# Optimization experiments

Measured on AMD Instinct MI355X. Metric: run time of the kernel, lower is better.

## Reference

```python
import jax, jax.numpy as jnp
import numpy as np

TEMPERATURE = 0.1
NEG_INF = -1e9


def setup_inputs() -> dict:
    key = jax.random.key(0)
    k1, k2 = jax.random.split(key)
    features = jax.random.normal(k1, (8192, 256), dtype=jnp.float32)
    labels = jax.random.randint(k2, (4096, 1), 0, 1000, dtype=jnp.int64)
    return {"features": features, "labels": labels}


def reference(features, labels):
    N = features.shape[0]
    n_views = N // labels.shape[0]
    # labels repeated over views: [N, 1]
    labels_nv = jnp.tile(labels, (n_views, 1))
    eye = jnp.eye(N, dtype=bool)
    # contrastive mask: 1 where same class, 0 on diagonal
    mask = (labels_nv == labels_nv.T).astype(features.dtype)
    mask = jnp.where(eye, 0.0, mask)
    # pairwise similarity logits [N, N], diagonal masked out
    logits = jnp.matmul(features, features.T) / TEMPERATURE
    logits = jnp.where(eye, NEG_INF, logits)
    # NOTE: torch code divides by mask.sum(dim=1) WITHOUT keepdim, which
    # broadcasts over the last axis (divide by column's row-sum). mask is
    # symmetric so this equals per-row normalization; replicate exactly.
    soft_label = mask / mask.sum(axis=1)
    log_proba = jax.nn.log_softmax(logits, axis=-1)
    loss_all = jnp.sum(soft_label * log_proba, axis=-1)  # [N]
    loss = -jnp.mean(loss_all) * TEMPERATURE
    return loss
```

## Files before the change

### kernel.cpp

```cpp
#include <hip/hip_runtime.h>

typedef __bf16 bf16_t;
typedef bf16_t bf16x8 __attribute__((ext_vector_type(8)));
typedef float f32x4 __attribute__((ext_vector_type(4)));
typedef unsigned short ushort_t;
typedef unsigned int uint_t;

#define C10L2E 14.4269504088896340736f
#define LN2    0.69314718055994530942f
#define NEG_BIG -3.0e38f
#define M0     -1.0e30f
#define THR_L2 11.5415603f

static __device__ __forceinline__ float fexp2(float x){ return __builtin_amdgcn_exp2f(x); }
static __device__ __forceinline__ float flog2(float x){ return __builtin_amdgcn_logf(x); }

#define GLOAD16(g, l) __builtin_amdgcn_global_load_lds( \
    (const __attribute__((address_space(1))) void*)(g), \
    (__attribute__((address_space(3))) void*)(l), 16, 0, 0)

#define WAITV(n) asm volatile("s_waitcnt vmcnt(" #n ")" ::: "memory")

static __device__ __forceinline__ ushort_t f2bf1(float f) {
    uint_t u = __float_as_uint(f);
    uint_t r = (u + 0x7fffu + ((u >> 16) & 1u)) >> 16;
    return (ushort_t)r;
}

__global__ void prep_kernel(const float* __restrict__ feat, const int* __restrict__ labels,
                            ushort_t* __restrict__ Fb, int* __restrict__ cnt,
                            int* __restrict__ idxl) {
    int i = blockIdx.x * 256 + threadIdx.x;
    float4 f = reinterpret_cast<const float4*>(feat)[i];
    ushort4 o;
    o.x = f2bf1(f.x); o.y = f2bf1(f.y); o.z = f2bf1(f.z); o.w = f2bf1(f.w);
    reinterpret_cast<ushort4*>(Fb)[i] = o;
    if (i < 4096) {
        int lab = labels[i];
        int p = atomicAdd(&cnt[lab], 1);
        if (p < 64) idxl[lab * 64 + p] = i;
    }
}

__global__ void classterm_kernel(const float* __restrict__ feat, const int* __restrict__ cnt,
                                 const int* __restrict__ idxl, float* __restrict__ term) {
    int c = blockIdx.x;
    int lane = threadIdx.x;
    int n = cnt[c];
    float4 g4 = make_float4(0.f, 0.f, 0.f, 0.f);
    float n2 = 0.f;
    for (int e = 0; e < n; ++e) {
        int r = idxl[c * 64 + e];
        float4 f0 = reinterpret_cast<const float4*>(feat)[(size_t)r * 64 + lane];
        float4 f1 = reinterpret_cast<const float4*>(feat)[(size_t)(r + 4096) * 64 + lane];
        g4.x += f0.x + f1.x; g4.y += f0.y + f1.y;
        g4.z += f0.z + f1.z; g4.w += f0.w + f1.w;
        n2 += f0.x*f0.x + f0.y*f0.y + f0.z*f0.z + f0.w*f0.w
            + f1.x*f1.x + f1.y*f1.y + f1.z*f1.z + f1.w*f1.w;
    }
    float gg = g4.x*g4.x + g4.y*g4.y + g4.z*g4.z + g4.w*g4.w;
    #pragma unroll
    for (int d = 1; d < 64; d <<= 1) {
        gg += __shfl_xor(gg, d, 64);
        n2 += __shfl_xor(n2, d, 64);
    }
    if (lane == 0) term[c] = (n > 0) ? (gg - n2) / (float)(2 * n - 1) : 0.0f;
}

__global__ __launch_bounds__(512, 1) void supcon_main(
        const ushort_t* __restrict__ Fb, float* __restrict__ part) {
    extern __shared__ char lds[];
    char* As = lds;
    char* Bb = lds + 65536;

    const int tid  = threadIdx.x;
    const int lane = tid & 63;
    const int wid  = tid >> 6;
    const int wr   = (wid >> 2) * 64;
    const int wc   = (wid & 3) * 64;
    const int g    = lane >> 4;
    const int l15  = lane & 15;
    const int r0 = blockIdx.x * 128;
    const int c0 = blockIdx.y * 2048;

    #pragma unroll
    for (int i = 0; i < 8; ++i) {
        int c = (wid * 8 + i) * 64 + lane;
        int row = c >> 5, sl = c & 31;
        int lslot = (sl & 16) | ((sl ^ row) & 15);
        GLOAD16(Fb + (size_t)(r0 + row) * 256 + lslot * 8, As + c * 16);
    }

    int bofs0, bofs1, bdst0, bdst1;
    {
        int c = tid;
        int col = c >> 2, pp = c & 3;
        bofs0 = col * 256 + (pp ^ ((col >> 1) & 3)) * 8;
        bdst0 = c * 16;
        c = 512 + tid;
        col = c >> 2; pp = c & 3;
        bofs1 = col * 256 + (pp ^ ((col >> 1) & 3)) * 8;
        bdst1 = c * 16;
    }
    auto stageB = [&](int p) {
        const ushort_t* base = Fb + (size_t)(c0 + (p >> 3) * 256) * 256 + (p & 7) * 32;
        char* Bd = Bb + (p & 3) * 16384;
        GLOAD16(base + bofs0, Bd + bdst0);
        GLOAD16(base + bofs1, Bd + bdst1);
    };

    stageB(0); stageB(1);

    float ML2[16], S[16];
    #pragma unroll
    for (int x = 0; x < 16; ++x) { ML2[x] = M0; S[x] = 0.0f; }

    f32x4 acc[4][4];

    #pragma unroll 1
    for (int t = 0; t < 8; ++t) {
        const int j0 = c0 + t * 256;
        #pragma unroll
        for (int e = 0; e < 8; ++e) {
            const int p = t * 8 + e;
            if (e <= 5) {
                stageB(p + 2);
                WAITV(4);
            } else if (e == 6) {
                if (t < 7) { stageB(p + 2); WAITV(4); } else { WAITV(2); }
            } else {
                if (t < 7) { stageB(p + 2); WAITV(4); } else { WAITV(0); }
            }
            __builtin_amdgcn_s_barrier();
            __builtin_amdgcn_sched_barrier(0);

            bf16x8 a[4], b[4];
            {
                int sA = e * 4 + g;
                int pA = (sA & 16) | ((sA ^ l15) & 15);
                #pragma unroll
                for (int m = 0; m < 4; ++m)
                    a[m] = *reinterpret_cast<const bf16x8*>(As + (wr + m * 16 + l15) * 512 + pA * 16);
                const char* Bp = Bb + (p & 3) * 16384;
                int pB = g ^ ((l15 >> 1) & 3);
                #pragma unroll
                for (int n = 0; n < 4; ++n)
                    b[n] = *reinterpret_cast<const bf16x8*>(Bp + (wc + n * 16 + l15) * 64 + pB * 16);
            }

            if (e == 0) {
                #pragma unroll
                for (int m = 0; m < 4; ++m)
                    #pragma unroll
                    for (int n = 0; n < 4; ++n)
                        #pragma unroll
                        for (int w = 0; w < 4; ++w) acc[m][n][w] = 0.0f;
            }
            #pragma unroll
            for (int m = 0; m < 4; ++m)
                #pragma unroll
                for (int n = 0; n < 4; ++n)
                    acc[m][n] = __builtin_amdgcn_mfma_f32_16x16x32_bf16(a[m], b[n], acc[m][n], 0, 0, 0);

            if (e == 7) {
                const bool diag = (j0 == (r0 & ~255));
                const int jc = j0 + wc + l15;
                #pragma unroll
                for (int m = 0; m < 4; ++m) {
                    #pragma unroll
                    for (int v = 0; v < 4; ++v) {
                        const int idx = m * 4 + v;
                        float x0 = acc[m][0][v], x1 = acc[m][1][v];
                        float x2 = acc[m][2][v], x3 = acc[m][3][v];
                        if (diag) {
                            int i = r0 + wr + m * 16 + g * 4 + v;
                            if (jc      == i) x0 = NEG_BIG;
                            if (jc + 16 == i) x1 = NEG_BIG;
                            if (jc + 32 == i) x2 = NEG_BIG;
                            if (jc + 48 == i) x3 = NEG_BIG;
                        }
                        float tm = fmaxf(fmaxf(x0, x1), fmaxf(x2, x3));
                        float cc = tm * C10L2E;
                        float ml = ML2[idx];
                        if (cc > ml + THR_L2) {
                            S[idx] *= fexp2(ml - cc);
                            ml = cc;
                            ML2[idx] = cc;
                        }
                        S[idx] += fexp2(fmaf(x0, C10L2E, -ml)) + fexp2(fmaf(x1, C10L2E, -ml))
                                + fexp2(fmaf(x2, C10L2E, -ml)) + fexp2(fmaf(x3, C10L2E, -ml));
                    }
                }
            }
        }
    }

    const int slot = blockIdx.y * 4 + (wid & 3);
    #pragma unroll
    for (int idx = 0; idx < 16; ++idx) {
        float m_ = ML2[idx], s_ = S[idx];
        #pragma unroll
        for (int d = 1; d < 16; d <<= 1) {
            float mo = __shfl_xor(m_, d, 64);
            float so = __shfl_xor(s_, d, 64);
            float nm = fmaxf(m_, mo);
            s_ = s_ * fexp2(m_ - nm) + so * fexp2(mo - nm);
            m_ = nm;
        }
        if (l15 == 0) {
            int i = r0 + wr + (idx >> 2) * 16 + g * 4 + (idx & 3);
            float2 val; val.x = m_; val.y = s_;
            *reinterpret_cast<float2*>(part + ((size_t)i * 16 + slot) * 2) = val;
        }
    }
}

__global__ void combine_kernel(const float* __restrict__ part, const float* __restrict__ term,
                               float* __restrict__ acc, int* __restrict__ cntr,
                               float* __restrict__ out) {
    __shared__ float sm[16];
    int tid = threadIdx.x;
    int row = blockIdx.x * 16 + (tid >> 4);
    int l16 = tid & 15;
    float2 v = reinterpret_cast<const float2*>(part)[(size_t)row * 16 + l16];
    float m_ = v.x, s_ = v.y;
    #pragma unroll
    for (int d = 1; d < 16; d <<= 1) {
        float mo = __shfl_xor(m_, d, 64);
        float so = __shfl_xor(s_, d, 64);
        float nm = fmaxf(m_, mo);
        s_ = s_ * fexp2(m_ - nm) + so * fexp2(mo - nm);
        m_ = nm;
    }
    if (l16 == 0) sm[tid >> 4] = LN2 * (m_ + flog2(s_));
    __syncthreads();
    if (tid == 0) {
        float a = 0.f;
        #pragma unroll
        for (int i = 0; i < 16; ++i) a += sm[i];
        a -= 10.0f * term[blockIdx.x];
        if (blockIdx.x < 488) a -= 10.0f * term[512 + blockIdx.x];
        atomicAdd(acc, a);
        __threadfence();
        int old = atomicAdd(cntr, 1);
        if (old == 511) {
            __threadfence();
            float tot = atomicAdd(acc, 0.0f);
            out[0] = tot * (0.1f / 8192.0f);
        }
    }
}

extern "C" void kernel_launch(void* const* d_in, const int* in_sizes, int n_in,
                              void* d_out, int out_size, void* d_ws, size_t ws_size,
                              hipStream_t stream) {
    const float* feat = (const float*)d_in[0];
    const int* labels = (const int*)d_in[1];
    float* out = (float*)d_out;

    char* ws = (char*)d_ws;
    ushort_t* Fb = (ushort_t*)ws;
    float* part  = (float*)(ws + (4u << 20));
    int* cnt     = (int*)(ws + (5u << 20));
    float* acc   = (float*)(ws + (5u << 20) + 4096);
    int* cntr    = (int*)(ws + (5u << 20) + 4100);
    int* idxl    = (int*)(ws + (5u << 20) + 8192);
    float* term  = (float*)(ws + (5u << 20) + 8192 + 262144);

    hipMemsetAsync(ws + (5u << 20), 0, 8192, stream);
    prep_kernel<<<2048, 256, 0, stream>>>(feat, labels, Fb, cnt, idxl);
    classterm_kernel<<<1000, 64, 0, stream>>>(feat, cnt, idxl, term);
    dim3 grid(64, 4);
    supcon_main<<<grid, 512, 131072, stream>>>(Fb, part);
    combine_kernel<<<512, 256, 0, stream>>>(part, term, acc, cntr, out);
}
```

Baseline: 80.89 us.

## Shrink main tile to 64 rows for two blocks per CU with triple-buffered B

The main GEMM+softmax kernel now uses 256-thread blocks covering 64 rows, with 4 waves each owning 64 columns. The grid doubles to 128x4 and LDS drops to 80KB, so two blocks can share a CU. B staging moves from four buffers to three and is issued after the barrier, with a simpler wait scheme. The A and B LDS swizzles are redone. The class-term kernel packs four classes per block. The aim is more occupancy and latency hiding, at the cost of reloading B twice as often from L2 and halving A reuse per block.

```diff
diff --git a/kernel.cpp b/kernel.cpp
--- a/kernel.cpp
+++ b/kernel.cpp
@@ -44,12 +44,12 @@
 
 __global__ void classterm_kernel(const float* __restrict__ feat, const int* __restrict__ cnt,
                                  const int* __restrict__ idxl, float* __restrict__ term) {
-    int c = blockIdx.x;
-    int lane = threadIdx.x;
+    int c = blockIdx.x * 4 + (threadIdx.x >> 6);
+    int lane = threadIdx.x & 63;
     int n = cnt[c];
     float4 g4 = make_float4(0.f, 0.f, 0.f, 0.f);
     float n2 = 0.f;
-    for (int e = 0; e < n; ++e) {
+    for (int e = 0; e < n && e < 64; ++e) {
         int r = idxl[c * 64 + e];
         float4 f0 = reinterpret_cast<const float4*>(feat)[(size_t)r * 64 + lane];
         float4 f1 = reinterpret_cast<const float4*>(feat)[(size_t)(r + 4096) * 64 + lane];
@@ -67,46 +67,44 @@
     if (lane == 0) term[c] = (n > 0) ? (gg - n2) / (float)(2 * n - 1) : 0.0f;
 }
 
-__global__ __launch_bounds__(512, 1) void supcon_main(
-        const ushort_t* __restrict__ Fb, float* __restrict__ part) {
+__global__ __launch_bounds__(256, 2) void supcon_main(
+        const ushort_t* __restrict__ Fb, float2* __restrict__ part) {
     extern __shared__ char lds[];
     char* As = lds;
-    char* Bb = lds + 65536;
+    char* Bb = lds + 32768;
 
     const int tid  = threadIdx.x;
     const int lane = tid & 63;
     const int wid  = tid >> 6;
-    const int wr   = (wid >> 2) * 64;
-    const int wc   = (wid & 3) * 64;
+    const int wcol = wid * 64;
     const int g    = lane >> 4;
     const int l15  = lane & 15;
-    const int r0 = blockIdx.x * 128;
+    const int r0 = blockIdx.x * 64;
     const int c0 = blockIdx.y * 2048;
 
     #pragma unroll
     for (int i = 0; i < 8; ++i) {
-        int c = (wid * 8 + i) * 64 + lane;
+        int c = i * 256 + tid;
         int row = c >> 5, sl = c & 31;
-        int lslot = (sl & 16) | ((sl ^ row) & 15);
-        GLOAD16(Fb + (size_t)(r0 + row) * 256 + lslot * 8, As + c * 16);
-    }
-
-    int bofs0, bofs1, bdst0, bdst1;
-    {
-        int c = tid;
-        int col = c >> 2, pp = c & 3;
-        bofs0 = col * 256 + (pp ^ ((col >> 1) & 3)) * 8;
-        bdst0 = c * 16;
-        c = 512 + tid;
-        col = c >> 2; pp = c & 3;
-        bofs1 = col * 256 + (pp ^ ((col >> 1) & 3)) * 8;
-        bdst1 = c * 16;
+        int s = sl ^ (row & 31);
+        GLOAD16(Fb + (size_t)(r0 + row) * 256 + s * 8, As + c * 16);
+    }
+
+    int bofs[4], bdst[4];
+    #pragma unroll
+    for (int i = 0; i < 4; ++i) {
+        int c = i * 256 + tid;
+        int col = c >> 2, sl = c & 3;
+        int s = sl ^ ((col >> 2) & 3);
+        bofs[i] = col * 256 + s * 8;
+        bdst[i] = c * 16;
     }
     auto stageB = [&](int p) {
         const ushort_t* base = Fb + (size_t)(c0 + (p >> 3) * 256) * 256 + (p & 7) * 32;
-        char* Bd = Bb + (p & 3) * 16384;
-        GLOAD16(base + bofs0, Bd + bdst0);
-        GLOAD16(base + bofs1, Bd + bdst1);
+        char* Bd = Bb + (p % 3) * 16384;
+        #pragma unroll
+        for (int i = 0; i < 4; ++i)
+            GLOAD16(base + bofs[i], Bd + bdst[i]);
     };
 
     stageB(0); stageB(1);
@@ -119,33 +117,28 @@
 
     #pragma unroll 1
     for (int t = 0; t < 8; ++t) {
-        const int j0 = c0 + t * 256;
         #pragma unroll
         for (int e = 0; e < 8; ++e) {
             const int p = t * 8 + e;
-            if (e <= 5) {
-                stageB(p + 2);
-                WAITV(4);
-            } else if (e == 6) {
-                if (t < 7) { stageB(p + 2); WAITV(4); } else { WAITV(2); }
-            } else {
-                if (t < 7) { stageB(p + 2); WAITV(4); } else { WAITV(0); }
-            }
+            if (p < 63) { WAITV(4); } else { WAITV(0); }
             __builtin_amdgcn_s_barrier();
             __builtin_amdgcn_sched_barrier(0);
+            if (p + 2 < 64) stageB(p + 2);
 
             bf16x8 a[4], b[4];
-            {
-                int sA = e * 4 + g;
-                int pA = (sA & 16) | ((sA ^ l15) & 15);
-                #pragma unroll
-                for (int m = 0; m < 4; ++m)
-                    a[m] = *reinterpret_cast<const bf16x8*>(As + (wr + m * 16 + l15) * 512 + pA * 16);
-                const char* Bp = Bb + (p & 3) * 16384;
-                int pB = g ^ ((l15 >> 1) & 3);
-                #pragma unroll
-                for (int n = 0; n < 4; ++n)
-                    b[n] = *reinterpret_cast<const bf16x8*>(Bp + (wc + n * 16 + l15) * 64 + pB * 16);
+            const int sA = e * 4 + g;
+            #pragma unroll
+            for (int m = 0; m < 4; ++m) {
+                int row = m * 16 + l15;
+                int phys = sA ^ (row & 31);
+                a[m] = *reinterpret_cast<const bf16x8*>(As + row * 512 + phys * 16);
+            }
+            const char* Bp = Bb + (p % 3) * 16384;
+            #pragma unroll
+            for (int n = 0; n < 4; ++n) {
+                int col = wcol + n * 16 + l15;
+                int phys = g ^ ((col >> 2) & 3);
+                b[n] = *reinterpret_cast<const bf16x8*>(Bp + col * 64 + phys * 16);
             }
 
             if (e == 0) {
@@ -163,8 +156,9 @@
                     acc[m][n] = __builtin_amdgcn_mfma_f32_16x16x32_bf16(a[m], b[n], acc[m][n], 0, 0, 0);
 
             if (e == 7) {
-                const bool diag = (j0 == (r0 & ~255));
-                const int jc = j0 + wc + l15;
+                const int jt = c0 + t * 256;
+                const bool diag = (jt == (r0 & ~255));
+                const int jc = jt + wcol + l15;
                 #pragma unroll
                 for (int m = 0; m < 4; ++m) {
                     #pragma unroll
@@ -173,7 +167,7 @@
                         float x0 = acc[m][0][v], x1 = acc[m][1][v];
                         float x2 = acc[m][2][v], x3 = acc[m][3][v];
                         if (diag) {
-                            int i = r0 + wr + m * 16 + g * 4 + v;
+                            int i = r0 + m * 16 + g * 4 + v;
                             if (jc      == i) x0 = NEG_BIG;
                             if (jc + 16 == i) x1 = NEG_BIG;
                             if (jc + 32 == i) x2 = NEG_BIG;
@@ -195,7 +189,7 @@
         }
     }
 
-    const int slot = blockIdx.y * 4 + (wid & 3);
+    const int slot = blockIdx.y * 4 + wid;
     #pragma unroll
     for (int idx = 0; idx < 16; ++idx) {
         float m_ = ML2[idx], s_ = S[idx];
@@ -208,21 +202,21 @@
             m_ = nm;
         }
         if (l15 == 0) {
-            int i = r0 + wr + (idx >> 2) * 16 + g * 4 + (idx & 3);
+            int i = r0 + (idx >> 2) * 16 + g * 4 + (idx & 3);
             float2 val; val.x = m_; val.y = s_;
-            *reinterpret_cast<float2*>(part + ((size_t)i * 16 + slot) * 2) = val;
-        }
-    }
-}
-
-__global__ void combine_kernel(const float* __restrict__ part, const float* __restrict__ term,
+            part[(size_t)i * 16 + slot] = val;
+        }
+    }
+}
+
+__global__ void combine_kernel(const float2* __restrict__ part, const float* __restrict__ term,
                                float* __restrict__ acc, int* __restrict__ cntr,
                                float* __restrict__ out) {
     __shared__ float sm[16];
     int tid = threadIdx.x;
     int row = blockIdx.x * 16 + (tid >> 4);
     int l16 = tid & 15;
-    float2 v = reinterpret_cast<const float2*>(part)[(size_t)row * 16 + l16];
+    float2 v = part[(size_t)row * 16 + l16];
     float m_ = v.x, s_ = v.y;
     #pragma unroll
     for (int d = 1; d < 16; d <<= 1) {
@@ -260,7 +254,7 @@
 
     char* ws = (char*)d_ws;
     ushort_t* Fb = (ushort_t*)ws;
-    float* part  = (float*)(ws + (4u << 20));
+    float2* part = (float2*)(ws + (4u << 20));
     int* cnt     = (int*)(ws + (5u << 20));
     float* acc   = (float*)(ws + (5u << 20) + 4096);
     int* cntr    = (int*)(ws + (5u << 20) + 4100);
@@ -269,8 +263,8 @@
 
     hipMemsetAsync(ws + (5u << 20), 0, 8192, stream);
     prep_kernel<<<2048, 256, 0, stream>>>(feat, labels, Fb, cnt, idxl);
-    classterm_kernel<<<1000, 64, 0, stream>>>(feat, cnt, idxl, term);
-    dim3 grid(64, 4);
-    supcon_main<<<grid, 512, 131072, stream>>>(Fb, part);
+    classterm_kernel<<<250, 256, 0, stream>>>(feat, cnt, idxl, term);
+    dim3 grid(128, 4);
+    supcon_main<<<grid, 256, 81920, stream>>>(Fb, part);
     combine_kernel<<<512, 256, 0, stream>>>(part, term, acc, cntr, out);
 }
```

Measured after the change: 92.18 us. +14.0%, slower.
